# Kernel optimization log

Hardware: AMD Instinct MI355X
Metric: run time of the kernel (lower is better)

Reference implementation:

```python
import jax, jax.numpy as jnp
import numpy as np

NUM_DRUGS, NUM_GENES = 20000, 40000
HIDDEN, HEADS, LAYERS = 128, 4, 2
D = HIDDEN // HEADS  # 32
E = 800000
BATCH = 4096


def setup_inputs() -> dict:
    key = jax.random.key(0)
    ks = jax.random.split(key, 26)
    f = lambda k, shape, s=0.05: jax.random.normal(k, shape, dtype=jnp.float32) * s
    ri = lambda k, shape, hi: jax.random.randint(k, shape, 0, hi, dtype=jnp.int32)
    inp = {
        'x_drug': f(ks[0], (NUM_DRUGS, HIDDEN), 1.0),
        'x_gene': f(ks[1], (NUM_GENES, HIDDEN), 1.0),
        # per-layer, per-node-type (0=drug, 1=gene) HGTConv linears
        'kW': f(ks[2], (LAYERS, 2, HIDDEN, HIDDEN)), 'kb': f(ks[3], (LAYERS, 2, HIDDEN)),
        'qW': f(ks[4], (LAYERS, 2, HIDDEN, HIDDEN)), 'qb': f(ks[5], (LAYERS, 2, HIDDEN)),
        'vW': f(ks[6], (LAYERS, 2, HIDDEN, HIDDEN)), 'vb': f(ks[7], (LAYERS, 2, HIDDEN)),
        'aW': f(ks[8], (LAYERS, 2, HIDDEN, HIDDEN)), 'ab': f(ks[9], (LAYERS, 2, HIDDEN)),
        'skip': f(ks[10], (LAYERS, 2), 1.0),
        # per-layer, per-edge-type (0 = drug->gene, 1 = gene->drug) relation params
        'a_rel': f(ks[11], (LAYERS, 2, HEADS, D, D)),
        'm_rel': f(ks[12], (LAYERS, 2, HEADS, D, D)),
        'p_rel': 1.0 + f(ks[13], (LAYERS, 2, HEADS), 0.1),
        # predictor MLP: Linear(256,128) -> ReLU -> Linear(128,1)
        'pW1': f(ks[14], (2 * HIDDEN, HIDDEN)), 'pb1': f(ks[15], (HIDDEN,)),
        'pW2': f(ks[16], (HIDDEN, 1)), 'pb2': f(ks[17], (1,)),
        'edge_dg_src': ri(ks[18], (E,), NUM_DRUGS),
        'edge_dg_dst': ri(ks[19], (E,), NUM_GENES),
        'edge_gd_src': ri(ks[20], (E,), NUM_GENES),
        'edge_gd_dst': ri(ks[21], (E,), NUM_DRUGS),
        'drug_idx': ri(ks[22], (BATCH,), NUM_DRUGS),
        'gene_idx': ri(ks[23], (BATCH,), NUM_GENES),  # unused by forward (per docstring)
    }
    return inp


def _rel_msg(k_src, v_src, q_dst, ar, mr, pr, src, dst, n_dst):
    # relation-specific key/value transforms: [N,H,D] x [H,D,D] -> [N,H,D]
    kr = jnp.einsum('nhd,hde->nhe', k_src, ar)
    vr = jnp.einsum('nhd,hde->nhe', v_src, mr)
    # edge-wise attention logits [E,H]
    alpha = (q_dst[dst] * kr[src]).sum(-1) * pr / np.sqrt(D)
    amax = jax.ops.segment_max(alpha, dst, num_segments=n_dst)
    a = jnp.exp(alpha - amax[dst])
    denom = jax.ops.segment_sum(a, dst, num_segments=n_dst)
    a = a / (denom[dst] + 1e-16)
    msg = vr[src] * a[:, :, None]  # [E,H,D]
    out = jax.ops.segment_sum(msg, dst, num_segments=n_dst)
    return out.reshape(n_dst, HIDDEN)


def _hgt_layer(xd, xg, kW, kb, qW, qb, vW, vb, aW, ab, skip, a_rel, m_rel, p_rel,
               dg_s, dg_d, gd_s, gd_d):
    proj = lambda x, W, b: (x @ W + b).reshape(x.shape[0], HEADS, D)
    kd, qd, vd = proj(xd, kW[0], kb[0]), proj(xd, qW[0], qb[0]), proj(xd, vW[0], vb[0])
    kg, qg, vg = proj(xg, kW[1], kb[1]), proj(xg, qW[1], qb[1]), proj(xg, vW[1], vb[1])
    # edge type 0: drug -> gene ; edge type 1: gene -> drug
    out_g = _rel_msg(kd, vd, qg, a_rel[0], m_rel[0], p_rel[0], dg_s, dg_d, NUM_GENES)
    out_d = _rel_msg(kg, vg, qd, a_rel[1], m_rel[1], p_rel[1], gd_s, gd_d, NUM_DRUGS)

    def finish(out, x, W, b, sk):
        out = jax.nn.gelu(out, approximate=False) @ W + b
        g = jax.nn.sigmoid(sk)
        return g * out + (1.0 - g) * x

    return (finish(out_d, xd, aW[0], ab[0], skip[0]),
            finish(out_g, xg, aW[1], ab[1], skip[1]))


def reference(x_drug, x_gene, kW, kb, qW, qb, vW, vb, aW, ab, skip, a_rel, m_rel, p_rel,
              pW1, pb1, pW2, pb2,
              edge_dg_src, edge_dg_dst, edge_gd_src, edge_gd_dst, drug_idx, gene_idx):
    xd, xg = x_drug, x_gene
    for l in range(LAYERS):
        xd, xg = _hgt_layer(xd, xg, kW[l], kb[l], qW[l], qb[l], vW[l], vb[l],
                            aW[l], ab[l], skip[l], a_rel[l], m_rel[l], p_rel[l],
                            edge_dg_src, edge_dg_dst, edge_gd_src, edge_gd_dst)
        xd, xg = jax.nn.relu(xd), jax.nn.relu(xg)
    drug_emb = xd[drug_idx]                                   # [B,128]
    gene_emb = jnp.broadcast_to(xg.mean(axis=0, keepdims=True),
                                (drug_idx.shape[0], HIDDEN))  # [B,128]
    comb = jnp.concatenate([drug_emb, gene_emb], axis=-1)     # [B,256]
    h = jax.nn.relu(comb @ pW1 + pb1)                         # dropout is eval no-op
    return (h @ pW2 + pb2).squeeze(-1)                        # [B]
```

## Files before the change

kernel.cpp:

```cpp
#include <hip/hip_runtime.h>
#include <hip/hip_bf16.h>
#include <math.h>

#define N_DRUG 20000
#define N_GENE 40000
#define HID 128
#define NEDGE 800000
#define NBATCH 4096

typedef unsigned short u16;
typedef unsigned int u32;
typedef __attribute__((ext_vector_type(8))) short short8;
typedef __attribute__((ext_vector_type(4))) float f32x4;

__device__ inline float gelu_exact(float x) {
    return 0.5f * x * (1.f + erff(x * 0.70710678118654752f));
}
__device__ inline u16 f2bf(float f) {
    u32 u = __float_as_uint(f);
    u += 0x7fffu + ((u >> 16) & 1u);
    return (u16)(u >> 16);
}
__device__ inline float bflo(u32 u) { return __uint_as_float(u << 16); }
__device__ inline float bfhi(u32 u) { return __uint_as_float(u & 0xffff0000u); }
__device__ inline float bf2f(u16 u) { return __uint_as_float(((u32)u) << 16); }
__device__ inline u32 pkbf(float a, float b) { return (u32)f2bf(a) | ((u32)f2bf(b) << 16); }

#define SWZ(row, kbyte) ((row) * 256 + ((kbyte) ^ (((row) & 7) << 4)))

__global__ void fuse_weights(const float* __restrict__ kW, const float* __restrict__ kb,
                             const float* __restrict__ qW, const float* __restrict__ qb,
                             const float* __restrict__ vW, const float* __restrict__ vb,
                             const float* __restrict__ a_rel, const float* __restrict__ m_rel,
                             const float* __restrict__ p_rel,
                             u16* __restrict__ BFt, float* __restrict__ BB) {
    int idx = blockIdx.x * 256 + threadIdx.x;
    if (idx >= 2 * 2 * 128 * 384) return;
    int j = idx % 384;
    int k = (idx / 384) % 128;
    int lt = idx / (384 * 128);
    const float rs = 0.17677669529663687f;
    float w, b;
    if (j < 128) {
        w = qW[(lt * 128 + k) * 128 + j];
        b = qb[lt * 128 + j];
    } else if (j < 256) {
        int c = j - 128, h = c >> 5, e = c & 31;
        float scale = p_rel[lt * 4 + h] * rs;
        const float* ar = a_rel + ((lt * 4 + h) * 32) * 32;
        const float* kWr = kW + (lt * 128 + k) * 128 + h * 32;
        const float* kbr = kb + lt * 128 + h * 32;
        float s = 0.f, sb = 0.f;
        for (int d = 0; d < 32; d++) { float a = ar[d * 32 + e]; s += kWr[d] * a; sb += kbr[d] * a; }
        w = s * scale; b = sb * scale;
    } else {
        int c = j - 256, h = c >> 5, e = c & 31;
        const float* mr = m_rel + ((lt * 4 + h) * 32) * 32;
        const float* vWr = vW + (lt * 128 + k) * 128 + h * 32;
        const float* vbr = vb + lt * 128 + h * 32;
        float s = 0.f, sb = 0.f;
        for (int d = 0; d < 32; d++) { float m = mr[d * 32 + e]; s += vWr[d] * m; sb += vbr[d] * m; }
        w = s; b = sb;
    }
    BFt[((size_t)lt * 384 + j) * 128 + k] = f2bf(w);
    if (k == 0) BB[lt * 384 + j] = b;
}

__global__ void prep_awt(const float* __restrict__ aW, u16* __restrict__ aWt) {
    int idx = blockIdx.x * 256 + threadIdx.x;
    if (idx >= 65536) return;
    int k = idx & 127, j = (idx >> 7) & 127, lt = idx >> 14;
    aWt[idx] = f2bf(aW[((size_t)lt * 128 + k) * 128 + j]);
}
__global__ void prep_w1at(const float* __restrict__ pW1, u16* __restrict__ W1at) {
    int idx = blockIdx.x * 256 + threadIdx.x;
    if (idx >= 16384) return;
    int k = idx & 127, j = idx >> 7;
    W1at[idx] = f2bf(pW1[(size_t)k * 128 + j]);
}

struct GArgs {
    const float* Af0; const float* Af1;
    const u16* Ab0;  const u16* Ab1;
    int N0; int N1; int gy0;
    const u16* Bt0;  const u16* Bt1;
    const float* bias0; const float* bias1;
    u16* QB0; u16* QB1;
    u16* KV0; u16* KV1;
    const float* skip0; const float* skip1;
    const float* Xc0; const float* Xc1;
    float* Xn0; float* Xn1;
    u16* Xb0; u16* Xb1;
    int afmt; int colTiles; int mode; int writeF32;
};

__global__ __launch_bounds__(256) void gemm_mfma(GArgs a) {
    __shared__ char As[128 * 256];
    __shared__ char Bs[64 * 256];
    const int tid = threadIdx.x;
    const int set = (blockIdx.y < (unsigned)a.gy0) ? 0 : 1;
    const int by = set ? (blockIdx.y - a.gy0) : blockIdx.y;
    const int rowBase = by * 128;
    const int N = set ? a.N1 : a.N0;
    const float* Af = set ? a.Af1 : a.Af0;
    const u16* Ab = set ? a.Ab1 : a.Ab0;
    const u16* Bt = set ? a.Bt1 : a.Bt0;
    const float* bias = set ? a.bias1 : a.bias0;
    u16* QB = set ? a.QB1 : a.QB0;
    u16* KV = set ? a.KV1 : a.KV0;
    const float* skipPtr = set ? a.skip1 : a.skip0;
    const float* Xcur = set ? a.Xc1 : a.Xc0;
    float* Xn = set ? a.Xn1 : a.Xn0;
    u16* Xb = set ? a.Xb1 : a.Xb0;

    if (a.afmt == 0) {
#pragma unroll
        for (int it = 0; it < 16; ++it) {
            int lin = it * 256 + tid;
            int row = lin >> 5, kq = lin & 31;
            int gr = rowBase + row;
            float4 av = make_float4(0.f, 0.f, 0.f, 0.f);
            if (gr < N) av = *(const float4*)(Af + (size_t)gr * 128 + kq * 4);
            uint2 p;
            p.x = pkbf(av.x, av.y);
            p.y = pkbf(av.z, av.w);
            *(uint2*)(As + SWZ(row, kq * 8)) = p;
        }
    } else {
#pragma unroll
        for (int it = 0; it < 8; ++it) {
            int lin = it * 256 + tid;
            int row = lin >> 4, kq = lin & 15;
            int gr = rowBase + row;
            uint4 v = make_uint4(0, 0, 0, 0);
            if (gr < N) v = *(const uint4*)(Ab + (size_t)gr * 128 + kq * 8);
            *(uint4*)(As + SWZ(row, kq * 16)) = v;
        }
    }

    const int w = tid >> 6, lane = tid & 63;
    const int r15 = lane & 15;
    const int klo = (lane >> 4) << 4;
    const int cq = (lane >> 4) << 2;
    float g = 0.f;
    if (a.mode == 1) g = 1.f / (1.f + expf(-skipPtr[0]));

    for (int ct = 0; ct < a.colTiles; ++ct) {
        const int colBase = (blockIdx.x * a.colTiles + ct) * 64;
        __syncthreads();
#pragma unroll
        for (int it = 0; it < 4; ++it) {
            int lin = it * 256 + tid;
            int j = lin >> 4, kq = lin & 15;
            uint4 v = *(const uint4*)(Bt + (size_t)(colBase + j) * 128 + kq * 8);
            *(uint4*)(Bs + SWZ(j, kq * 16)) = v;
        }
        __syncthreads();

        f32x4 acc[2][4];
#pragma unroll
        for (int mt = 0; mt < 2; ++mt)
#pragma unroll
            for (int nt = 0; nt < 4; ++nt) acc[mt][nt] = (f32x4){0.f, 0.f, 0.f, 0.f};

#pragma unroll
        for (int kb = 0; kb < 4; ++kb) {
            int kbyte = kb * 64 + klo;
            short8 af[2], bf[4];
#pragma unroll
            for (int mt = 0; mt < 2; ++mt) {
                int row = w * 32 + mt * 16 + r15;
                af[mt] = *(short8*)(As + SWZ(row, kbyte));
            }
#pragma unroll
            for (int nt = 0; nt < 4; ++nt) {
                int col = nt * 16 + r15;
                bf[nt] = *(short8*)(Bs + SWZ(col, kbyte));
            }
#pragma unroll
            for (int mt = 0; mt < 2; ++mt)
#pragma unroll
                for (int nt = 0; nt < 4; ++nt)
                    acc[mt][nt] = __builtin_amdgcn_mfma_f32_16x16x32_bf16(bf[nt], af[mt], acc[mt][nt], 0, 0, 0);
        }

#pragma unroll
        for (int mt = 0; mt < 2; ++mt) {
            int grow = rowBase + w * 32 + mt * 16 + r15;
            if (grow >= N) continue;
#pragma unroll
            for (int nt = 0; nt < 4; ++nt) {
                int col = colBase + nt * 16 + cq;
                float4 bi = *(const float4*)(bias + col);
                float v0 = acc[mt][nt][0] + bi.x;
                float v1 = acc[mt][nt][1] + bi.y;
                float v2 = acc[mt][nt][2] + bi.z;
                float v3 = acc[mt][nt][3] + bi.w;
                if (a.mode == 2) {
                    uint2 p; p.x = pkbf(v0, v1); p.y = pkbf(v2, v3);
                    if (col < 128) {
                        *(uint2*)(QB + (size_t)grow * 128 + col) = p;
                    } else if (col < 256) {
                        *(uint2*)(KV + (size_t)grow * 256 + (col - 128)) = p;
                    } else {
                        *(uint2*)(KV + (size_t)grow * 256 + 128 + (col - 256)) = p;
                    }
                } else {
                    float4 xv = *(const float4*)(Xcur + (size_t)grow * 128 + col);
                    float o0 = fmaxf(g * v0 + (1.f - g) * xv.x, 0.f);
                    float o1 = fmaxf(g * v1 + (1.f - g) * xv.y, 0.f);
                    float o2 = fmaxf(g * v2 + (1.f - g) * xv.z, 0.f);
                    float o3 = fmaxf(g * v3 + (1.f - g) * xv.w, 0.f);
                    if (a.writeF32)
                        *(float4*)(Xn + (size_t)grow * 128 + col) = make_float4(o0, o1, o2, o3);
                    uint2 p; p.x = pkbf(o0, o1); p.y = pkbf(o2, o3);
                    *(uint2*)(Xb + (size_t)grow * 128 + col) = p;
                }
            }
        }
    }
}

__global__ void hist2(const int* __restrict__ d0, int* __restrict__ c0,
                      const int* __restrict__ d1, int* __restrict__ c1, int gridE) {
    int b = blockIdx.x;
    const int* d; int* c; int bb;
    if (b < gridE) { d = d0; c = c0; bb = b; } else { d = d1; c = c1; bb = b - gridE; }
    int e = bb * 256 + threadIdx.x;
    if (e < NEDGE) atomicAdd(c + d[e], 1);
}

#define SCAN_NBG 10
#define SCAN_NBD 5
__global__ __launch_bounds__(256) void scan_local(const int* __restrict__ cntG,
                                                  const int* __restrict__ cntD,
                                                  int* __restrict__ outG, int* __restrict__ outD,
                                                  int* __restrict__ bsum) {
    __shared__ int tmp[256];
    int b = blockIdx.x, t = threadIdx.x;
    const int* cnt; int* out; int n; int cbase;
    if (b < SCAN_NBG) { cnt = cntG; out = outG; n = N_GENE; cbase = b * 4096; }
    else { cnt = cntD; out = outD; n = N_DRUG; cbase = (b - SCAN_NBG) * 4096; }
    int base = cbase + t * 16;
    int v[16], s = 0;
#pragma unroll
    for (int i = 0; i < 16; ++i) { int idx = base + i; v[i] = (idx < n) ? cnt[idx] : 0; s += v[i]; }
    tmp[t] = s;
    __syncthreads();
    for (int off = 1; off < 256; off <<= 1) {
        int add = (t >= off) ? tmp[t - off] : 0;
        __syncthreads();
        tmp[t] += add;
        __syncthreads();
    }
    int run = tmp[t] - s;
#pragma unroll
    for (int i = 0; i < 16; ++i) { int idx = base + i; if (idx < n) out[idx] = run; run += v[i]; }
    if (t == 255) bsum[b] = tmp[255];
}

__global__ void scan_bsum(int* __restrict__ bsum) {
    if (threadIdx.x == 0) {
        int run = 0;
        for (int i = 0; i < SCAN_NBG; ++i) { int v = bsum[i]; bsum[i] = run; run += v; }
        run = 0;
        for (int i = SCAN_NBG; i < SCAN_NBG + SCAN_NBD; ++i) { int v = bsum[i]; bsum[i] = run; run += v; }
    }
}

__global__ __launch_bounds__(256) void scan_add(int* __restrict__ outG, int* __restrict__ outD,
                                                const int* __restrict__ bsum) {
    int b = blockIdx.x, t = threadIdx.x;
    int* out; int n; int cbase;
    if (b < SCAN_NBG) { out = outG; n = N_GENE; cbase = b * 4096; }
    else { out = outD; n = N_DRUG; cbase = (b - SCAN_NBG) * 4096; }
    int o = bsum[b];
    int base = cbase + t * 16;
#pragma unroll
    for (int i = 0; i < 16; ++i) { int idx = base + i; if (idx < n) out[idx] += o; }
    if (t == 0 && b == SCAN_NBG - 1) outG[N_GENE] = NEDGE;
    if (t == 0 && b == SCAN_NBG + SCAN_NBD - 1) outD[N_DRUG] = NEDGE;
}

__global__ void scatter2(const int* __restrict__ s0, const int* __restrict__ d0,
                         const int* __restrict__ r0, int* __restrict__ cur0, int* __restrict__ o0,
                         const int* __restrict__ s1, const int* __restrict__ d1,
                         const int* __restrict__ r1, int* __restrict__ cur1, int* __restrict__ o1,
                         int gridE) {
    int b = blockIdx.x;
    const int *src, *dst, *row; int *cursor, *outp; int bb;
    if (b < gridE) { src = s0; dst = d0; row = r0; cursor = cur0; outp = o0; bb = b; }
    else { src = s1; dst = d1; row = r1; cursor = cur1; outp = o1; bb = b - gridE; }
    int e = bb * 256 + threadIdx.x;
    if (e < NEDGE) {
        int d = dst[e];
        int pos = row[d] + atomicSub(cursor + d, 1) - 1;
        outp[pos] = src[e];
    }
}

__global__ __launch_bounds__(256) void fused_attn(const int* __restrict__ rowG,
                                                  const int* __restrict__ srcG,
                                                  const u16* __restrict__ QGB,
                                                  const u16* __restrict__ KVD,
                                                  u16* __restrict__ NUMG,
                                                  const int* __restrict__ rowD,
                                                  const int* __restrict__ srcD,
                                                  const u16* __restrict__ QDB,
                                                  const u16* __restrict__ KVG,
                                                  u16* __restrict__ NUMD) {
    int node = (blockIdx.x * 256 + threadIdx.x) >> 6;
    int lane = threadIdx.x & 63;
    const int* rowStart; const int* srcSorted; const u16* Qb; const u16* KV; u16* out; int nd;
    if (node < N_GENE) { rowStart = rowG; srcSorted = srcG; Qb = QGB; KV = KVD; out = NUMG; nd = node; }
    else if (node < N_GENE + N_DRUG) { rowStart = rowD; srcSorted = srcD; Qb = QDB; KV = KVG; out = NUMD; nd = node - N_GENE; }
    else return;
    const int g = lane >> 4;
    const int sl = lane & 15;

    float qr[8];
    {
        uint4 qv = *(const uint4*)(Qb + (size_t)nd * 128 + sl * 8);
        qr[0] = bflo(qv.x); qr[1] = bfhi(qv.x);
        qr[2] = bflo(qv.y); qr[3] = bfhi(qv.y);
        qr[4] = bflo(qv.z); qr[5] = bfhi(qv.z);
        qr[6] = bflo(qv.w); qr[7] = bfhi(qv.w);
    }
    int beg = rowStart[nd], end = rowStart[nd + 1];
    float s = 0.f;
    float acc[8] = {0.f, 0.f, 0.f, 0.f, 0.f, 0.f, 0.f, 0.f};

#define FETCH(t, kk, vv)                                                \
    {                                                                   \
        int sid = __shfl(sids, 4 * (t) + g);                            \
        const u16* rowp = KV + ((size_t)sid << 8);                      \
        kk = *(const uint4*)(rowp + sl * 8);                            \
        vv = *(const uint4*)(rowp + 128 + sl * 8);                      \
    }
#define COMPUTE(t, kk, vv)                                              \
    {                                                                   \
        float part = qr[0] * bflo(kk.x) + qr[1] * bfhi(kk.x)            \
                   + qr[2] * bflo(kk.y) + qr[3] * bfhi(kk.y)            \
                   + qr[4] * bflo(kk.z) + qr[5] * bfhi(kk.z)            \
                   + qr[6] * bflo(kk.w) + qr[7] * bfhi(kk.w);           \
        part += __shfl_xor(part, 1);                                    \
        part += __shfl_xor(part, 2);                                    \
        float a = (base + 4 * (t) + g < end) ? __expf(part) : 0.f;      \
        s += a;                                                         \
        acc[0] += a * bflo(vv.x); acc[1] += a * bfhi(vv.x);             \
        acc[2] += a * bflo(vv.y); acc[3] += a * bfhi(vv.y);             \
        acc[4] += a * bflo(vv.z); acc[5] += a * bfhi(vv.z);             \
        acc[6] += a * bflo(vv.w); acc[7] += a * bfhi(vv.w);             \
    }

    for (int base = beg; base < end; base += 64) {
        int bn = end - base; if (bn > 64) bn = 64;
        int ld = base + lane; if (ld > end - 1) ld = end - 1;
        int sids = srcSorted[ld];
        int nIter = (bn + 3) >> 2;
        uint4 k0, v0, k1, v1;
        FETCH(0, k0, v0);
        for (int t = 0; t < nIter; t += 2) {
            if (t + 1 < nIter) FETCH(t + 1, k1, v1);
            COMPUTE(t, k0, v0);
            if (t + 1 >= nIter) break;
            if (t + 2 < nIter) FETCH(t + 2, k0, v0);
            COMPUTE(t + 1, k1, v1);
        }
    }
#undef FETCH
#undef COMPUTE

    s += __shfl_xor(s, 16);
    s += __shfl_xor(s, 32);
#pragma unroll
    for (int j = 0; j < 8; ++j) {
        acc[j] += __shfl_xor(acc[j], 16);
        acc[j] += __shfl_xor(acc[j], 32);
    }
    if (lane < 16) {
        float inv = 1.f / (s + 1e-16f);
        float r0 = gelu_exact(acc[0] * inv), r1 = gelu_exact(acc[1] * inv);
        float r2 = gelu_exact(acc[2] * inv), r3 = gelu_exact(acc[3] * inv);
        float r4 = gelu_exact(acc[4] * inv), r5 = gelu_exact(acc[5] * inv);
        float r6 = gelu_exact(acc[6] * inv), r7 = gelu_exact(acc[7] * inv);
        uint4 o;
        o.x = pkbf(r0, r1); o.y = pkbf(r2, r3); o.z = pkbf(r4, r5); o.w = pkbf(r6, r7);
        *(uint4*)(out + (size_t)nd * 128 + sl * 8) = o;
    }
}

__global__ __launch_bounds__(128) void colsum_bf(const u16* __restrict__ X, int N,
                                                 float* __restrict__ out) {
    int c = threadIdx.x;
    float s = 0.f;
    for (int r = blockIdx.x; r < N; r += gridDim.x) s += bf2f(X[(size_t)r * 128 + c]);
    atomicAdd(out + c, s);
}

__global__ __launch_bounds__(128) void c2_kernel(const float* __restrict__ gsum,
                                                 const float* __restrict__ pW1,
                                                 const float* __restrict__ pb1,
                                                 float* __restrict__ c2) {
    int j = threadIdx.x;
    float s = pb1[j];
    for (int k = 0; k < 128; ++k)
        s += gsum[k] * (1.f / 40000.f) * pW1[(size_t)(128 + k) * 128 + j];
    c2[j] = s;
}

__global__ __launch_bounds__(256) void predictor_mfma(const u16* __restrict__ Xdb,
                                                      const int* __restrict__ didx,
                                                      const u16* __restrict__ W1at,
                                                      const float* __restrict__ c2,
                                                      const float* __restrict__ pW2,
                                                      const float* __restrict__ pb2,
                                                      float* __restrict__ out) {
    __shared__ char As[128 * 256];
    __shared__ char Bs[128 * 256];
    const int tid = threadIdx.x;
    const int rowBase = blockIdx.x * 128;

#pragma unroll
    for (int it = 0; it < 8; ++it) {
        int lin = it * 256 + tid;
        int row = lin >> 4, kq = lin & 15;
        int dn = didx[rowBase + row];
        uint4 v = *(const uint4*)(Xdb + (size_t)dn * 128 + kq * 8);
        *(uint4*)(As + SWZ(row, kq * 16)) = v;
        uint4 wv = *(const uint4*)(W1at + (size_t)row * 128 + kq * 8);
        *(uint4*)(Bs + SWZ(row, kq * 16)) = wv;
    }
    __syncthreads();

    const int w = tid >> 6, lane = tid & 63;
    const int r15 = lane & 15;
    const int klo = (lane >> 4) << 4;
    f32x4 acc[2][8];
#pragma unroll
    for (int mt = 0; mt < 2; ++mt)
#pragma unroll
        for (int nt = 0; nt < 8; ++nt) acc[mt][nt] = (f32x4){0.f, 0.f, 0.f, 0.f};

#pragma unroll
    for (int kb = 0; kb < 4; ++kb) {
        int kbyte = kb * 64 + klo;
        short8 af[2], bf[8];
#pragma unroll
        for (int mt = 0; mt < 2; ++mt) af[mt] = *(short8*)(As + SWZ(w * 32 + mt * 16 + r15, kbyte));
#pragma unroll
        for (int nt = 0; nt < 8; ++nt) bf[nt] = *(short8*)(Bs + SWZ(nt * 16 + r15, kbyte));
#pragma unroll
        for (int mt = 0; mt < 2; ++mt)
#pragma unroll
            for (int nt = 0; nt < 8; ++nt)
                acc[mt][nt] = __builtin_amdgcn_mfma_f32_16x16x32_bf16(af[mt], bf[nt], acc[mt][nt], 0, 0, 0);
    }

    float c2v[8], w2v[8];
#pragma unroll
    for (int nt = 0; nt < 8; ++nt) {
        int col = nt * 16 + r15;
        c2v[nt] = c2[col];
        w2v[nt] = pW2[col];
    }
    float bias2 = pb2[0];
#pragma unroll
    for (int mt = 0; mt < 2; ++mt) {
#pragma unroll
        for (int r = 0; r < 4; ++r) {
            float rsum = 0.f;
#pragma unroll
            for (int nt = 0; nt < 8; ++nt)
                rsum += fmaxf(acc[mt][nt][r] + c2v[nt], 0.f) * w2v[nt];
            rsum += __shfl_xor(rsum, 1);
            rsum += __shfl_xor(rsum, 2);
            rsum += __shfl_xor(rsum, 4);
            rsum += __shfl_xor(rsum, 8);
            if (r15 == 0)
                out[rowBase + w * 32 + mt * 16 + ((lane >> 4) << 2) + r] = rsum + bias2;
        }
    }
}

extern "C" void kernel_launch(void* const* d_in, const int* in_sizes, int n_in,
                              void* d_out, int out_size, void* d_ws, size_t ws_size,
                              hipStream_t stream) {
    const float* x_drug = (const float*)d_in[0];
    const float* x_gene = (const float*)d_in[1];
    const float* kW = (const float*)d_in[2];
    const float* kb = (const float*)d_in[3];
    const float* qW = (const float*)d_in[4];
    const float* qb = (const float*)d_in[5];
    const float* vW = (const float*)d_in[6];
    const float* vb = (const float*)d_in[7];
    const float* aW = (const float*)d_in[8];
    const float* ab = (const float*)d_in[9];
    const float* skip = (const float*)d_in[10];
    const float* a_rel = (const float*)d_in[11];
    const float* m_rel = (const float*)d_in[12];
    const float* p_rel = (const float*)d_in[13];
    const float* pW1 = (const float*)d_in[14];
    const float* pb1 = (const float*)d_in[15];
    const float* pW2 = (const float*)d_in[16];
    const float* pb2 = (const float*)d_in[17];
    const int* e_dg_s = (const int*)d_in[18];
    const int* e_dg_d = (const int*)d_in[19];
    const int* e_gd_s = (const int*)d_in[20];
    const int* e_gd_d = (const int*)d_in[21];
    const int* drug_idx = (const int*)d_in[22];

    char* base = (char*)d_ws;
    size_t off = 0;
    auto alloc = [&](size_t bytes) { char* p = base + off; off += (bytes + 255) & ~(size_t)255; return p; };
    u16*   QDB  = (u16*)alloc((size_t)N_DRUG * 128 * 2);
    u16*   QGB  = (u16*)alloc((size_t)N_GENE * 128 * 2);
    u16*   KVD  = (u16*)alloc((size_t)N_DRUG * 256 * 2);
    u16*   KVG  = (u16*)alloc((size_t)N_GENE * 256 * 2);
    float* XD0  = (float*)alloc((size_t)N_DRUG * 128 * 4);
    float* XG0  = (float*)alloc((size_t)N_GENE * 128 * 4);
    u16*   XDb  = (u16*)alloc((size_t)N_DRUG * 128 * 2);
    u16*   XGb  = (u16*)alloc((size_t)N_GENE * 128 * 2);
    u16*   NUMD = (u16*)alloc((size_t)N_DRUG * 128 * 2);
    u16*   NUMG = (u16*)alloc((size_t)N_GENE * 128 * 2);
    u16*   BFt  = (u16*)alloc((size_t)2 * 2 * 384 * 128 * 2);
    float* BB   = (float*)alloc((size_t)2 * 2 * 384 * 4);
    u16*   aWt  = (u16*)alloc((size_t)2 * 2 * 128 * 128 * 2);
    u16*   W1at = (u16*)alloc((size_t)128 * 128 * 2);
    float* GSUM = (float*)alloc(128 * 4);
    float* C2   = (float*)alloc(128 * 4);
    int* rowG = (int*)alloc(40001 * 4);
    int* rowD = (int*)alloc(20001 * 4);
    int* cntG = (int*)alloc(40000 * 4);
    int* cntD = (int*)alloc(20000 * 4);
    int* bsum = (int*)alloc(64 * 4);
    int* srcG = (int*)alloc((size_t)NEDGE * 4);
    int* srcD = (int*)alloc((size_t)NEDGE * 4);

    fuse_weights<<<768, 256, 0, stream>>>(kW, kb, qW, qb, vW, vb, a_rel, m_rel, p_rel, BFt, BB);
    prep_awt<<<256, 256, 0, stream>>>(aW, aWt);
    prep_w1at<<<64, 256, 0, stream>>>(pW1, W1at);

    const int gridE = (NEDGE + 255) / 256;
    hipMemsetAsync(cntG, 0, 40000 * sizeof(int), stream);
    hipMemsetAsync(cntD, 0, 20000 * sizeof(int), stream);
    hist2<<<2 * gridE, 256, 0, stream>>>(e_dg_d, cntG, e_gd_d, cntD, gridE);
    scan_local<<<SCAN_NBG + SCAN_NBD, 256, 0, stream>>>(cntG, cntD, rowG, rowD, bsum);
    scan_bsum<<<1, 64, 0, stream>>>(bsum);
    scan_add<<<SCAN_NBG + SCAN_NBD, 256, 0, stream>>>(rowG, rowD, bsum);
    scatter2<<<2 * gridE, 256, 0, stream>>>(e_dg_s, e_dg_d, rowG, cntG, srcG,
                                            e_gd_s, e_gd_d, rowD, cntD, srcD, gridE);

    const int gyD = (N_DRUG + 127) / 128;
    const int gyG = (N_GENE + 127) / 128;
    const int gyT = gyD + gyG;

    const float* xd_cur = x_drug;
    const float* xg_cur = x_gene;

    for (int l = 0; l < 2; ++l) {
        GArgs qa = {};
        qa.Af0 = xd_cur; qa.Af1 = xg_cur;
        qa.Ab0 = XDb;    qa.Ab1 = XGb;
        qa.N0 = N_DRUG;  qa.N1 = N_GENE; qa.gy0 = gyD;
        qa.Bt0 = BFt + (size_t)(l * 2 + 0) * 384 * 128;
        qa.Bt1 = BFt + (size_t)(l * 2 + 1) * 384 * 128;
        qa.bias0 = BB + (size_t)(l * 2 + 0) * 384;
        qa.bias1 = BB + (size_t)(l * 2 + 1) * 384;
        qa.QB0 = QDB; qa.QB1 = QGB; qa.KV0 = KVD; qa.KV1 = KVG;
        qa.afmt = (l == 0) ? 0 : 1; qa.colTiles = 3; qa.mode = 2; qa.writeF32 = 0;
        gemm_mfma<<<dim3(2, gyT), 256, 0, stream>>>(qa);

        fused_attn<<<(N_GENE + N_DRUG + 3) / 4, 256, 0, stream>>>(
            rowG, srcG, QGB, KVD, NUMG, rowD, srcD, QDB, KVG, NUMD);

        GArgs oa = {};
        oa.Ab0 = NUMD; oa.Ab1 = NUMG;
        oa.N0 = N_DRUG; oa.N1 = N_GENE; oa.gy0 = gyD;
        oa.Bt0 = aWt + (size_t)(l * 2 + 0) * 16384;
        oa.Bt1 = aWt + (size_t)(l * 2 + 1) * 16384;
        oa.bias0 = ab + (size_t)(l * 2 + 0) * 128;
        oa.bias1 = ab + (size_t)(l * 2 + 1) * 128;
        oa.skip0 = skip + (l * 2 + 0); oa.skip1 = skip + (l * 2 + 1);
        oa.Xc0 = xd_cur; oa.Xc1 = xg_cur;
        oa.Xn0 = XD0; oa.Xn1 = XG0;
        oa.Xb0 = XDb; oa.Xb1 = XGb;
        oa.afmt = 1; oa.colTiles = 2; oa.mode = 1; oa.writeF32 = (l == 0) ? 1 : 0;
        gemm_mfma<<<dim3(1, gyT), 256, 0, stream>>>(oa);

        xd_cur = XD0;
        xg_cur = XG0;
    }

    hipMemsetAsync(GSUM, 0, 128 * sizeof(float), stream);
    colsum_bf<<<256, 128, 0, stream>>>(XGb, N_GENE, GSUM);
    c2_kernel<<<1, 128, 0, stream>>>(GSUM, pW1, pb1, C2);
    predictor_mfma<<<NBATCH / 128, 256, 0, stream>>>(XDb, drug_idx, W1at, C2, pW2, pb2, (float*)d_out);
}
```

Baseline: 525.0 us.

## Fuse layer-1 output projection with layer-2 QKV GEMM and fold prologue kernels

Merges the three weight-prep kernels and the counter memsets into one prologue launch. Fuses the layer-1 output projection, skip and ReLU with the layer-2 QKV GEMM, keeping the intermediate bf16 tile in shared memory instead of reloading it from global. The final gene column mean is computed as per-block partial sums in the last GEMM epilogue, which removes the colsum and c2 kernels and the bf16 gene buffer; the predictor reduces the partials itself. The scan_bsum pass is folded into scan_add2. The aim is fewer launches and less global traffic, at the cost of a heavier fused kernel with more registers and redundant c2 work in every predictor block.

```diff
diff --git a/kernel.cpp b/kernel.cpp
--- a/kernel.cpp
+++ b/kernel.cpp
@@ -23,60 +23,62 @@
 }
 __device__ inline float bflo(u32 u) { return __uint_as_float(u << 16); }
 __device__ inline float bfhi(u32 u) { return __uint_as_float(u & 0xffff0000u); }
-__device__ inline float bf2f(u16 u) { return __uint_as_float(((u32)u) << 16); }
 __device__ inline u32 pkbf(float a, float b) { return (u32)f2bf(a) | ((u32)f2bf(b) << 16); }
 
 #define SWZ(row, kbyte) ((row) * 256 + ((kbyte) ^ (((row) & 7) << 4)))
 
-__global__ void fuse_weights(const float* __restrict__ kW, const float* __restrict__ kb,
-                             const float* __restrict__ qW, const float* __restrict__ qb,
-                             const float* __restrict__ vW, const float* __restrict__ vb,
-                             const float* __restrict__ a_rel, const float* __restrict__ m_rel,
-                             const float* __restrict__ p_rel,
-                             u16* __restrict__ BFt, float* __restrict__ BB) {
-    int idx = blockIdx.x * 256 + threadIdx.x;
-    if (idx >= 2 * 2 * 128 * 384) return;
-    int j = idx % 384;
-    int k = (idx / 384) % 128;
-    int lt = idx / (384 * 128);
-    const float rs = 0.17677669529663687f;
-    float w, b;
-    if (j < 128) {
-        w = qW[(lt * 128 + k) * 128 + j];
-        b = qb[lt * 128 + j];
-    } else if (j < 256) {
-        int c = j - 128, h = c >> 5, e = c & 31;
-        float scale = p_rel[lt * 4 + h] * rs;
-        const float* ar = a_rel + ((lt * 4 + h) * 32) * 32;
-        const float* kWr = kW + (lt * 128 + k) * 128 + h * 32;
-        const float* kbr = kb + lt * 128 + h * 32;
-        float s = 0.f, sb = 0.f;
-        for (int d = 0; d < 32; d++) { float a = ar[d * 32 + e]; s += kWr[d] * a; sb += kbr[d] * a; }
-        w = s * scale; b = sb * scale;
+__global__ __launch_bounds__(256) void prologue(const float* __restrict__ kW, const float* __restrict__ kb,
+                                                const float* __restrict__ qW, const float* __restrict__ qb,
+                                                const float* __restrict__ vW, const float* __restrict__ vb,
+                                                const float* __restrict__ a_rel, const float* __restrict__ m_rel,
+                                                const float* __restrict__ p_rel,
+                                                const float* __restrict__ aW, const float* __restrict__ pW1,
+                                                u16* __restrict__ BFt, float* __restrict__ BB,
+                                                u16* __restrict__ aWt, u16* __restrict__ W1at,
+                                                int* __restrict__ cnt) {
+    int b = blockIdx.x, tid = threadIdx.x;
+    if (b < 768) {
+        int idx = b * 256 + tid;
+        int j = idx % 384;
+        int k = (idx / 384) % 128;
+        int lt = idx / (384 * 128);
+        const float rs = 0.17677669529663687f;
+        float w, bb;
+        if (j < 128) {
+            w = qW[(lt * 128 + k) * 128 + j];
+            bb = qb[lt * 128 + j];
+        } else if (j < 256) {
+            int c = j - 128, h = c >> 5, e = c & 31;
+            float scale = p_rel[lt * 4 + h] * rs;
+            const float* ar = a_rel + ((lt * 4 + h) * 32) * 32;
+            const float* kWr = kW + (lt * 128 + k) * 128 + h * 32;
+            const float* kbr = kb + lt * 128 + h * 32;
+            float s = 0.f, sb = 0.f;
+            for (int d = 0; d < 32; d++) { float a = ar[d * 32 + e]; s += kWr[d] * a; sb += kbr[d] * a; }
+            w = s * scale; bb = sb * scale;
+        } else {
+            int c = j - 256, h = c >> 5, e = c & 31;
+            const float* mr = m_rel + ((lt * 4 + h) * 32) * 32;
+            const float* vWr = vW + (lt * 128 + k) * 128 + h * 32;
+            const float* vbr = vb + lt * 128 + h * 32;
+            float s = 0.f, sb = 0.f;
+            for (int d = 0; d < 32; d++) { float m = mr[d * 32 + e]; s += vWr[d] * m; sb += vbr[d] * m; }
+            w = s; bb = sb;
+        }
+        BFt[((size_t)lt * 384 + j) * 128 + k] = f2bf(w);
+        if (k == 0) BB[lt * 384 + j] = bb;
+    } else if (b < 1024) {
+        int idx = (b - 768) * 256 + tid;
+        int k = idx & 127, j = (idx >> 7) & 127, lt = idx >> 14;
+        aWt[idx] = f2bf(aW[((size_t)lt * 128 + k) * 128 + j]);
+    } else if (b < 1088) {
+        int idx = (b - 1024) * 256 + tid;
+        int k = idx & 127, j = idx >> 7;
+        W1at[idx] = f2bf(pW1[(size_t)k * 128 + j]);
     } else {
-        int c = j - 256, h = c >> 5, e = c & 31;
-        const float* mr = m_rel + ((lt * 4 + h) * 32) * 32;
-        const float* vWr = vW + (lt * 128 + k) * 128 + h * 32;
-        const float* vbr = vb + lt * 128 + h * 32;
-        float s = 0.f, sb = 0.f;
-        for (int d = 0; d < 32; d++) { float m = mr[d * 32 + e]; s += vWr[d] * m; sb += vbr[d] * m; }
-        w = s; b = sb;
-    }
-    BFt[((size_t)lt * 384 + j) * 128 + k] = f2bf(w);
-    if (k == 0) BB[lt * 384 + j] = b;
-}
-
-__global__ void prep_awt(const float* __restrict__ aW, u16* __restrict__ aWt) {
-    int idx = blockIdx.x * 256 + threadIdx.x;
-    if (idx >= 65536) return;
-    int k = idx & 127, j = (idx >> 7) & 127, lt = idx >> 14;
-    aWt[idx] = f2bf(aW[((size_t)lt * 128 + k) * 128 + j]);
-}
-__global__ void prep_w1at(const float* __restrict__ pW1, u16* __restrict__ W1at) {
-    int idx = blockIdx.x * 256 + threadIdx.x;
-    if (idx >= 16384) return;
-    int k = idx & 127, j = idx >> 7;
-    W1at[idx] = f2bf(pW1[(size_t)k * 128 + j]);
+        int idx = (b - 1088) * 256 + tid;
+        if (idx < 60000) cnt[idx] = 0;
+    }
 }
 
 struct GArgs {
@@ -91,12 +93,14 @@
     const float* Xc0; const float* Xc1;
     float* Xn0; float* Xn1;
     u16* Xb0; u16* Xb1;
+    float* colPart;
     int afmt; int colTiles; int mode; int writeF32;
 };
 
 __global__ __launch_bounds__(256) void gemm_mfma(GArgs a) {
     __shared__ char As[128 * 256];
     __shared__ char Bs[64 * 256];
+    __shared__ float sums[4][128];
     const int tid = threadIdx.x;
     const int set = (blockIdx.y < (unsigned)a.gy0) ? 0 : 1;
     const int by = set ? (blockIdx.y - a.gy0) : blockIdx.y;
@@ -112,6 +116,7 @@
     const float* Xcur = set ? a.Xc1 : a.Xc0;
     float* Xn = set ? a.Xn1 : a.Xn0;
     u16* Xb = set ? a.Xb1 : a.Xb0;
+    const bool doCol = (a.mode == 1) && (set == 1) && (a.colPart != nullptr);
 
     if (a.afmt == 0) {
 #pragma unroll
@@ -168,15 +173,11 @@
             int kbyte = kb * 64 + klo;
             short8 af[2], bf[4];
 #pragma unroll
-            for (int mt = 0; mt < 2; ++mt) {
-                int row = w * 32 + mt * 16 + r15;
-                af[mt] = *(short8*)(As + SWZ(row, kbyte));
-            }
-#pragma unroll
-            for (int nt = 0; nt < 4; ++nt) {
-                int col = nt * 16 + r15;
-                bf[nt] = *(short8*)(Bs + SWZ(col, kbyte));
-            }
+            for (int mt = 0; mt < 2; ++mt)
+                af[mt] = *(short8*)(As + SWZ(w * 32 + mt * 16 + r15, kbyte));
+#pragma unroll
+            for (int nt = 0; nt < 4; ++nt)
+                bf[nt] = *(short8*)(Bs + SWZ(nt * 16 + r15, kbyte));
 #pragma unroll
             for (int mt = 0; mt < 2; ++mt)
 #pragma unroll
@@ -185,13 +186,14 @@
         }
 
 #pragma unroll
-        for (int mt = 0; mt < 2; ++mt) {
-            int grow = rowBase + w * 32 + mt * 16 + r15;
-            if (grow >= N) continue;
-#pragma unroll
-            for (int nt = 0; nt < 4; ++nt) {
-                int col = colBase + nt * 16 + cq;
-                float4 bi = *(const float4*)(bias + col);
+        for (int nt = 0; nt < 4; ++nt) {
+            int col = colBase + nt * 16 + cq;
+            float4 bi = *(const float4*)(bias + col);
+            float c0 = 0.f, c1 = 0.f, c2 = 0.f, c3 = 0.f;
+#pragma unroll
+            for (int mt = 0; mt < 2; ++mt) {
+                int grow = rowBase + w * 32 + mt * 16 + r15;
+                if (grow >= N) continue;
                 float v0 = acc[mt][nt][0] + bi.x;
                 float v1 = acc[mt][nt][1] + bi.y;
                 float v2 = acc[mt][nt][2] + bi.z;
@@ -213,11 +215,188 @@
                     float o3 = fmaxf(g * v3 + (1.f - g) * xv.w, 0.f);
                     if (a.writeF32)
                         *(float4*)(Xn + (size_t)grow * 128 + col) = make_float4(o0, o1, o2, o3);
-                    uint2 p; p.x = pkbf(o0, o1); p.y = pkbf(o2, o3);
-                    *(uint2*)(Xb + (size_t)grow * 128 + col) = p;
+                    if (Xb) {
+                        uint2 p; p.x = pkbf(o0, o1); p.y = pkbf(o2, o3);
+                        *(uint2*)(Xb + (size_t)grow * 128 + col) = p;
+                    }
+                    c0 += o0; c1 += o1; c2 += o2; c3 += o3;
                 }
             }
-        }
+            if (doCol) {
+#pragma unroll
+                for (int sft = 1; sft <= 8; sft <<= 1) {
+                    c0 += __shfl_xor(c0, sft);
+                    c1 += __shfl_xor(c1, sft);
+                    c2 += __shfl_xor(c2, sft);
+                    c3 += __shfl_xor(c3, sft);
+                }
+                if (r15 == 0) {
+                    int lcol = colBase + nt * 16 + cq;
+                    *(float4*)&sums[w][lcol] = make_float4(c0, c1, c2, c3);
+                }
+            }
+        }
+    }
+    if (doCol) {
+        __syncthreads();
+        if (tid < 128) {
+            float p = sums[0][tid] + sums[1][tid] + sums[2][tid] + sums[3][tid];
+            a.colPart[(size_t)by * 128 + tid] = p;
+        }
+    }
+}
+
+__global__ __launch_bounds__(256) void fused_out_qkv(const u16* __restrict__ NUMD, const u16* __restrict__ NUMG,
+                                                     const u16* __restrict__ aWt, const float* __restrict__ ab,
+                                                     const float* __restrict__ skip,
+                                                     const float* __restrict__ xd, const float* __restrict__ xg,
+                                                     float* __restrict__ XD0, float* __restrict__ XG0,
+                                                     const u16* __restrict__ BFt, const float* __restrict__ BB,
+                                                     u16* __restrict__ QDB, u16* __restrict__ QGB,
+                                                     u16* __restrict__ KVD, u16* __restrict__ KVG, int gy0) {
+    __shared__ char As[128 * 256];
+    __shared__ char Bs[64 * 256];
+    const int tid = threadIdx.x;
+    const int set = (blockIdx.x < (unsigned)gy0) ? 0 : 1;
+    const int by = set ? (blockIdx.x - gy0) : blockIdx.x;
+    const int rowBase = by * 128;
+    const int N = set ? N_GENE : N_DRUG;
+    const u16* A = set ? NUMG : NUMD;
+    const u16* W1 = aWt + (size_t)set * 16384;
+    const float* b1 = ab + (size_t)set * 128;
+    const float* Xc = set ? xg : xd;
+    float* Xn = set ? XG0 : XD0;
+    const u16* B2 = BFt + (size_t)(2 + set) * 384 * 128;
+    const float* bb2 = BB + (size_t)(2 + set) * 384;
+    u16* QB = set ? QGB : QDB;
+    u16* KV = set ? KVG : KVD;
+    const float g = 1.f / (1.f + expf(-skip[set]));
+
+#pragma unroll
+    for (int it = 0; it < 8; ++it) {
+        int lin = it * 256 + tid;
+        int row = lin >> 4, kq = lin & 15;
+        int gr = rowBase + row;
+        uint4 v = make_uint4(0, 0, 0, 0);
+        if (gr < N) v = *(const uint4*)(A + (size_t)gr * 128 + kq * 8);
+        *(uint4*)(As + SWZ(row, kq * 16)) = v;
+    }
+    __syncthreads();
+
+    const int w = tid >> 6, lane = tid & 63;
+    const int r15 = lane & 15;
+    const int klo = (lane >> 4) << 4;
+    const int cq = (lane >> 4) << 2;
+
+    f32x4 acc1[2][2][4];
+#pragma unroll
+    for (int ct = 0; ct < 2; ++ct) {
+#pragma unroll
+        for (int it = 0; it < 4; ++it) {
+            int lin = it * 256 + tid;
+            int j = lin >> 4, kq = lin & 15;
+            uint4 v = *(const uint4*)(W1 + (size_t)(ct * 64 + j) * 128 + kq * 8);
+            *(uint4*)(Bs + SWZ(j, kq * 16)) = v;
+        }
+        __syncthreads();
+#pragma unroll
+        for (int mt = 0; mt < 2; ++mt)
+#pragma unroll
+            for (int nt = 0; nt < 4; ++nt) acc1[ct][mt][nt] = (f32x4){0.f, 0.f, 0.f, 0.f};
+#pragma unroll
+        for (int kb = 0; kb < 4; ++kb) {
+            int kbyte = kb * 64 + klo;
+            short8 af[2], bf[4];
+#pragma unroll
+            for (int mt = 0; mt < 2; ++mt)
+                af[mt] = *(short8*)(As + SWZ(w * 32 + mt * 16 + r15, kbyte));
+#pragma unroll
+            for (int nt = 0; nt < 4; ++nt)
+                bf[nt] = *(short8*)(Bs + SWZ(nt * 16 + r15, kbyte));
+#pragma unroll
+            for (int mt = 0; mt < 2; ++mt)
+#pragma unroll
+                for (int nt = 0; nt < 4; ++nt)
+                    acc1[ct][mt][nt] = __builtin_amdgcn_mfma_f32_16x16x32_bf16(bf[nt], af[mt], acc1[ct][mt][nt], 0, 0, 0);
+        }
+        __syncthreads();
+    }
+#pragma unroll
+    for (int ct = 0; ct < 2; ++ct) {
+#pragma unroll
+        for (int nt = 0; nt < 4; ++nt) {
+            int col = ct * 64 + nt * 16 + cq;
+            float4 bi = *(const float4*)(b1 + col);
+#pragma unroll
+            for (int mt = 0; mt < 2; ++mt) {
+                int row = w * 32 + mt * 16 + r15;
+                int grow = rowBase + row;
+                if (grow >= N) continue;
+                float4 xv = *(const float4*)(Xc + (size_t)grow * 128 + col);
+                float o0 = fmaxf(g * (acc1[ct][mt][nt][0] + bi.x) + (1.f - g) * xv.x, 0.f);
+                float o1 = fmaxf(g * (acc1[ct][mt][nt][1] + bi.y) + (1.f - g) * xv.y, 0.f);
+                float o2 = fmaxf(g * (acc1[ct][mt][nt][2] + bi.z) + (1.f - g) * xv.z, 0.f);
+                float o3 = fmaxf(g * (acc1[ct][mt][nt][3] + bi.w) + (1.f - g) * xv.w, 0.f);
+                *(float4*)(Xn + (size_t)grow * 128 + col) = make_float4(o0, o1, o2, o3);
+                uint2 p; p.x = pkbf(o0, o1); p.y = pkbf(o2, o3);
+                *(uint2*)(As + SWZ(row, col * 2)) = p;
+            }
+        }
+    }
+
+    for (int ct2 = 0; ct2 < 6; ++ct2) {
+#pragma unroll
+        for (int it = 0; it < 4; ++it) {
+            int lin = it * 256 + tid;
+            int j = lin >> 4, kq = lin & 15;
+            uint4 v = *(const uint4*)(B2 + (size_t)(ct2 * 64 + j) * 128 + kq * 8);
+            *(uint4*)(Bs + SWZ(j, kq * 16)) = v;
+        }
+        __syncthreads();
+        f32x4 acc[2][4];
+#pragma unroll
+        for (int mt = 0; mt < 2; ++mt)
+#pragma unroll
+            for (int nt = 0; nt < 4; ++nt) acc[mt][nt] = (f32x4){0.f, 0.f, 0.f, 0.f};
+#pragma unroll
+        for (int kb = 0; kb < 4; ++kb) {
+            int kbyte = kb * 64 + klo;
+            short8 af[2], bf[4];
+#pragma unroll
+            for (int mt = 0; mt < 2; ++mt)
+                af[mt] = *(short8*)(As + SWZ(w * 32 + mt * 16 + r15, kbyte));
+#pragma unroll
+            for (int nt = 0; nt < 4; ++nt)
+                bf[nt] = *(short8*)(Bs + SWZ(nt * 16 + r15, kbyte));
+#pragma unroll
+            for (int mt = 0; mt < 2; ++mt)
+#pragma unroll
+                for (int nt = 0; nt < 4; ++nt)
+                    acc[mt][nt] = __builtin_amdgcn_mfma_f32_16x16x32_bf16(bf[nt], af[mt], acc[mt][nt], 0, 0, 0);
+        }
+#pragma unroll
+        for (int nt = 0; nt < 4; ++nt) {
+            int col = ct2 * 64 + nt * 16 + cq;
+            float4 bi = *(const float4*)(bb2 + col);
+#pragma unroll
+            for (int mt = 0; mt < 2; ++mt) {
+                int grow = rowBase + w * 32 + mt * 16 + r15;
+                if (grow >= N) continue;
+                float v0 = acc[mt][nt][0] + bi.x;
+                float v1 = acc[mt][nt][1] + bi.y;
+                float v2 = acc[mt][nt][2] + bi.z;
+                float v3 = acc[mt][nt][3] + bi.w;
+                uint2 p; p.x = pkbf(v0, v1); p.y = pkbf(v2, v3);
+                if (col < 128) {
+                    *(uint2*)(QB + (size_t)grow * 128 + col) = p;
+                } else if (col < 256) {
+                    *(uint2*)(KV + (size_t)grow * 256 + (col - 128)) = p;
+                } else {
+                    *(uint2*)(KV + (size_t)grow * 256 + 128 + (col - 256)) = p;
+                }
+            }
+        }
+        __syncthreads();
     }
 }
 
@@ -259,22 +438,17 @@
     if (t == 255) bsum[b] = tmp[255];
 }
 
-__global__ void scan_bsum(int* __restrict__ bsum) {
-    if (threadIdx.x == 0) {
-        int run = 0;
-        for (int i = 0; i < SCAN_NBG; ++i) { int v = bsum[i]; bsum[i] = run; run += v; }
-        run = 0;
-        for (int i = SCAN_NBG; i < SCAN_NBG + SCAN_NBD; ++i) { int v = bsum[i]; bsum[i] = run; run += v; }
-    }
-}
-
-__global__ __launch_bounds__(256) void scan_add(int* __restrict__ outG, int* __restrict__ outD,
-                                                const int* __restrict__ bsum) {
+__global__ __launch_bounds__(256) void scan_add2(int* __restrict__ outG, int* __restrict__ outD,
+                                                 const int* __restrict__ bsum) {
     int b = blockIdx.x, t = threadIdx.x;
-    int* out; int n; int cbase;
-    if (b < SCAN_NBG) { out = outG; n = N_GENE; cbase = b * 4096; }
-    else { out = outD; n = N_DRUG; cbase = (b - SCAN_NBG) * 4096; }
-    int o = bsum[b];
+    int* out; int n; int cbase; int o = 0;
+    if (b < SCAN_NBG) {
+        out = outG; n = N_GENE; cbase = b * 4096;
+        for (int i = 0; i < b; ++i) o += bsum[i];
+    } else {
+        out = outD; n = N_DRUG; cbase = (b - SCAN_NBG) * 4096;
+        for (int i = SCAN_NBG; i < b; ++i) o += bsum[i];
+    }
     int base = cbase + t * 16;
 #pragma unroll
     for (int i = 0; i < 16; ++i) { int idx = base + i; if (idx < n) out[idx] += o; }
@@ -345,7 +519,7 @@
                    + qr[6] * bflo(kk.w) + qr[7] * bfhi(kk.w);           \
         part += __shfl_xor(part, 1);                                    \
         part += __shfl_xor(part, 2);                                    \
-        float a = (base + 4 * (t) + g < end) ? __expf(part) : 0.f;      \
+        float a = ((t) < tm) ? __expf(part) : 0.f;                      \
         s += a;                                                         \
         acc[0] += a * bflo(vv.x); acc[1] += a * bfhi(vv.x);             \
         acc[2] += a * bflo(vv.y); acc[3] += a * bfhi(vv.y);             \
@@ -358,6 +532,7 @@
         int ld = base + lane; if (ld > end - 1) ld = end - 1;
         int sids = srcSorted[ld];
         int nIter = (bn + 3) >> 2;
+        int tm = (bn - g + 3) >> 2;
         uint4 k0, v0, k1, v1;
         FETCH(0, k0, v0);
         for (int t = 0; t < nIter; t += 2) {
@@ -378,46 +553,30 @@
         acc[j] += __shfl_xor(acc[j], 16);
         acc[j] += __shfl_xor(acc[j], 32);
     }
-    if (lane < 16) {
-        float inv = 1.f / (s + 1e-16f);
-        float r0 = gelu_exact(acc[0] * inv), r1 = gelu_exact(acc[1] * inv);
-        float r2 = gelu_exact(acc[2] * inv), r3 = gelu_exact(acc[3] * inv);
-        float r4 = gelu_exact(acc[4] * inv), r5 = gelu_exact(acc[5] * inv);
-        float r6 = gelu_exact(acc[6] * inv), r7 = gelu_exact(acc[7] * inv);
-        uint4 o;
-        o.x = pkbf(r0, r1); o.y = pkbf(r2, r3); o.z = pkbf(r4, r5); o.w = pkbf(r6, r7);
-        *(uint4*)(out + (size_t)nd * 128 + sl * 8) = o;
-    }
-}
-
-__global__ __launch_bounds__(128) void colsum_bf(const u16* __restrict__ X, int N,
-                                                 float* __restrict__ out) {
-    int c = threadIdx.x;
-    float s = 0.f;
-    for (int r = blockIdx.x; r < N; r += gridDim.x) s += bf2f(X[(size_t)r * 128 + c]);
-    atomicAdd(out + c, s);
-}
-
-__global__ __launch_bounds__(128) void c2_kernel(const float* __restrict__ gsum,
-                                                 const float* __restrict__ pW1,
-                                                 const float* __restrict__ pb1,
-                                                 float* __restrict__ c2) {
-    int j = threadIdx.x;
-    float s = pb1[j];
-    for (int k = 0; k < 128; ++k)
-        s += gsum[k] * (1.f / 40000.f) * pW1[(size_t)(128 + k) * 128 + j];
-    c2[j] = s;
+    float inv = 1.f / (s + 1e-16f);
+    float a0, a1;
+    if (g == 0)      { a0 = acc[0]; a1 = acc[1]; }
+    else if (g == 1) { a0 = acc[2]; a1 = acc[3]; }
+    else if (g == 2) { a0 = acc[4]; a1 = acc[5]; }
+    else             { a0 = acc[6]; a1 = acc[7]; }
+    float r0 = gelu_exact(a0 * inv);
+    float r1 = gelu_exact(a1 * inv);
+    *(u32*)(out + (size_t)nd * 128 + sl * 8 + 2 * g) = pkbf(r0, r1);
 }
 
 __global__ __launch_bounds__(256) void predictor_mfma(const u16* __restrict__ Xdb,
                                                       const int* __restrict__ didx,
                                                       const u16* __restrict__ W1at,
-                                                      const float* __restrict__ c2,
+                                                      const float* __restrict__ colPart, int nParts,
+                                                      const float* __restrict__ pW1,
+                                                      const float* __restrict__ pb1,
                                                       const float* __restrict__ pW2,
                                                       const float* __restrict__ pb2,
                                                       float* __restrict__ out) {
     __shared__ char As[128 * 256];
     __shared__ char Bs[128 * 256];
+    __shared__ float gsL[128];
+    __shared__ float c2s[128];
     const int tid = threadIdx.x;
     const int rowBase = blockIdx.x * 128;
 
@@ -431,6 +590,17 @@
         uint4 wv = *(const uint4*)(W1at + (size_t)row * 128 + kq * 8);
         *(uint4*)(Bs + SWZ(row, kq * 16)) = wv;
     }
+    if (tid < 128) {
+        float sum = 0.f;
+        for (int b = 0; b < nParts; ++b) sum += colPart[(size_t)b * 128 + tid];
+        gsL[tid] = sum * (1.f / 40000.f);
+    }
+    __syncthreads();
+    if (tid < 128) {
+        float s = pb1[tid];
+        for (int k = 0; k < 128; ++k) s += gsL[k] * pW1[(size_t)(128 + k) * 128 + tid];
+        c2s[tid] = s;
+    }
     __syncthreads();
 
     const int w = tid >> 6, lane = tid & 63;
@@ -461,7 +631,7 @@
 #pragma unroll
     for (int nt = 0; nt < 8; ++nt) {
         int col = nt * 16 + r15;
-        c2v[nt] = c2[col];
+        c2v[nt] = c2s[col];
         w2v[nt] = pW2[col];
     }
     float bias2 = pb2[0];
@@ -510,6 +680,10 @@
     const int* e_gd_d = (const int*)d_in[21];
     const int* drug_idx = (const int*)d_in[22];
 
+    const int gyD = (N_DRUG + 127) / 128;
+    const int gyG = (N_GENE + 127) / 128;
+    const int gyT = gyD + gyG;
+
     char* base = (char*)d_ws;
     size_t off = 0;
     auto alloc = [&](size_t bytes) { char* p = base + off; off += (bytes + 255) & ~(size_t)255; return p; };
@@ -520,15 +694,13 @@
     float* XD0  = (float*)alloc((size_t)N_DRUG * 128 * 4);
     float* XG0  = (float*)alloc((size_t)N_GENE * 128 * 4);
     u16*   XDb  = (u16*)alloc((size_t)N_DRUG * 128 * 2);
-    u16*   XGb  = (u16*)alloc((size_t)N_GENE * 128 * 2);
     u16*   NUMD = (u16*)alloc((size_t)N_DRUG * 128 * 2);
     u16*   NUMG = (u16*)alloc((size_t)N_GENE * 128 * 2);
     u16*   BFt  = (u16*)alloc((size_t)2 * 2 * 384 * 128 * 2);
     float* BB   = (float*)alloc((size_t)2 * 2 * 384 * 4);
     u16*   aWt  = (u16*)alloc((size_t)2 * 2 * 128 * 128 * 2);
     u16*   W1at = (u16*)alloc((size_t)128 * 128 * 2);
-    float* GSUM = (float*)alloc(128 * 4);
-    float* C2   = (float*)alloc(128 * 4);
+    float* colPart = (float*)alloc((size_t)gyG * 128 * 4);
     int* rowG = (int*)alloc(40001 * 4);
     int* rowD = (int*)alloc(20001 * 4);
     int* cntG = (int*)alloc(40000 * 4);
@@ -537,63 +709,46 @@
     int* srcG = (int*)alloc((size_t)NEDGE * 4);
     int* srcD = (int*)alloc((size_t)NEDGE * 4);
 
-    fuse_weights<<<768, 256, 0, stream>>>(kW, kb, qW, qb, vW, vb, a_rel, m_rel, p_rel, BFt, BB);
-    prep_awt<<<256, 256, 0, stream>>>(aW, aWt);
-    prep_w1at<<<64, 256, 0, stream>>>(pW1, W1at);
+    prologue<<<1323, 256, 0, stream>>>(kW, kb, qW, qb, vW, vb, a_rel, m_rel, p_rel,
+                                       aW, pW1, BFt, BB, aWt, W1at, cntG);
 
     const int gridE = (NEDGE + 255) / 256;
-    hipMemsetAsync(cntG, 0, 40000 * sizeof(int), stream);
-    hipMemsetAsync(cntD, 0, 20000 * sizeof(int), stream);
     hist2<<<2 * gridE, 256, 0, stream>>>(e_dg_d, cntG, e_gd_d, cntD, gridE);
     scan_local<<<SCAN_NBG + SCAN_NBD, 256, 0, stream>>>(cntG, cntD, rowG, rowD, bsum);
-    scan_bsum<<<1, 64, 0, stream>>>(bsum);
-    scan_add<<<SCAN_NBG + SCAN_NBD, 256, 0, stream>>>(rowG, rowD, bsum);
+    scan_add2<<<SCAN_NBG + SCAN_NBD, 256, 0, stream>>>(rowG, rowD, bsum);
     scatter2<<<2 * gridE, 256, 0, stream>>>(e_dg_s, e_dg_d, rowG, cntG, srcG,
                                             e_gd_s, e_gd_d, rowD, cntD, srcD, gridE);
 
-    const int gyD = (N_DRUG + 127) / 128;
-    const int gyG = (N_GENE + 127) / 128;
-    const int gyT = gyD + gyG;
-
-    const float* xd_cur = x_drug;
-    const float* xg_cur = x_gene;
-
-    for (int l = 0; l < 2; ++l) {
-        GArgs qa = {};
-        qa.Af0 = xd_cur; qa.Af1 = xg_cur;
-        qa.Ab0 = XDb;    qa.Ab1 = XGb;
-        qa.N0 = N_DRUG;  qa.N1 = N_GENE; qa.gy0 = gyD;
-        qa.Bt0 = BFt + (size_t)(l * 2 + 0) * 384 * 128;
-        qa.Bt1 = BFt + (size_t)(l * 2 + 1) * 384 * 128;
-        qa.bias0 = BB + (size_t)(l * 2 + 0) * 384;
-        qa.bias1 = BB + (size_t)(l * 2 + 1) * 384;
-        qa.QB0 = QDB; qa.QB1 = QGB; qa.KV0 = KVD; qa.KV1 = KVG;
-        qa.afmt = (l == 0) ? 0 : 1; qa.colTiles = 3; qa.mode = 2; qa.writeF32 = 0;
-        gemm_mfma<<<dim3(2, gyT), 256, 0, stream>>>(qa);
-
-        fused_attn<<<(N_GENE + N_DRUG + 3) / 4, 256, 0, stream>>>(
-            rowG, srcG, QGB, KVD, NUMG, rowD, srcD, QDB, KVG, NUMD);
-
-        GArgs oa = {};
-        oa.Ab0 = NUMD; oa.Ab1 = NUMG;
-        oa.N0 = N_DRUG; oa.N1 = N_GENE; oa.gy0 = gyD;
-        oa.Bt0 = aWt + (size_t)(l * 2 + 0) * 16384;
-        oa.Bt1 = aWt + (size_t)(l * 2 + 1) * 16384;
-        oa.bias0 = ab + (size_t)(l * 2 + 0) * 128;
-        oa.bias1 = ab + (size_t)(l * 2 + 1) * 128;
-        oa.skip0 = skip + (l * 2 + 0); oa.skip1 = skip + (l * 2 + 1);
-        oa.Xc0 = xd_cur; oa.Xc1 = xg_cur;
-        oa.Xn0 = XD0; oa.Xn1 = XG0;
-        oa.Xb0 = XDb; oa.Xb1 = XGb;
-        oa.afmt = 1; oa.colTiles = 2; oa.mode = 1; oa.writeF32 = (l == 0) ? 1 : 0;
-        gemm_mfma<<<dim3(1, gyT), 256, 0, stream>>>(oa);
-
-        xd_cur = XD0;
-        xg_cur = XG0;
-    }
-
-    hipMemsetAsync(GSUM, 0, 128 * sizeof(float), stream);
-    colsum_bf<<<256, 128, 0, stream>>>(XGb, N_GENE, GSUM);
-    c2_kernel<<<1, 128, 0, stream>>>(GSUM, pW1, pb1, C2);
-    predictor_mfma<<<NBATCH / 128, 256, 0, stream>>>(XDb, drug_idx, W1at, C2, pW2, pb2, (float*)d_out);
-}
+    GArgs qa = {};
+    qa.Af0 = x_drug; qa.Af1 = x_gene;
+    qa.N0 = N_DRUG;  qa.N1 = N_GENE; qa.gy0 = gyD;
+    qa.Bt0 = BFt;                    qa.Bt1 = BFt + (size_t)1 * 384 * 128;
+    qa.bias0 = BB;                   qa.bias1 = BB + 384;
+    qa.QB0 = QDB; qa.QB1 = QGB; qa.KV0 = KVD; qa.KV1 = KVG;
+    qa.afmt = 0; qa.colTiles = 3; qa.mode = 2; qa.writeF32 = 0;
+    gemm_mfma<<<dim3(2, gyT), 256, 0, stream>>>(qa);
+
+    fused_attn<<<(N_GENE + N_DRUG + 3) / 4, 256, 0, stream>>>(
+        rowG, srcG, QGB, KVD, NUMG, rowD, srcD, QDB, KVG, NUMD);
+
+    fused_out_qkv<<<gyT, 256, 0, stream>>>(NUMD, NUMG, aWt, ab, skip, x_drug, x_gene,
+                                           XD0, XG0, BFt, BB, QDB, QGB, KVD, KVG, gyD);
+
+    fused_attn<<<(N_GENE + N_DRUG + 3) / 4, 256, 0, stream>>>(
+        rowG, srcG, QGB, KVD, NUMG, rowD, srcD, QDB, KVG, NUMD);
+
+    GArgs oa = {};
+    oa.Ab0 = NUMD; oa.Ab1 = NUMG;
+    oa.N0 = N_DRUG; oa.N1 = N_GENE; oa.gy0 = gyD;
+    oa.Bt0 = aWt + (size_t)2 * 16384; oa.Bt1 = aWt + (size_t)3 * 16384;
+    oa.bias0 = ab + 2 * 128;          oa.bias1 = ab + 3 * 128;
+    oa.skip0 = skip + 2;              oa.skip1 = skip + 3;
+    oa.Xc0 = XD0; oa.Xc1 = XG0;
+    oa.Xb0 = XDb; oa.Xb1 = nullptr;
+    oa.colPart = colPart;
+    oa.afmt = 1; oa.colTiles = 2; oa.mode = 1; oa.writeF32 = 0;
+    gemm_mfma<<<dim3(1, gyT), 256, 0, stream>>>(oa);
+
+    predictor_mfma<<<NBATCH / 128, 256, 0, stream>>>(XDb, drug_idx, W1at, colPart, gyG,
+                                                     pW1, pb1, pW2, pb2, (float*)d_out);
+}
```

After: 512.9 us. 2.3% less time.
